# Kernel tuning notes

Measured on AMD Instinct MI355X. Metric: run time of the kernel, lower is better.

Reference implementation:

```python
import jax, jax.numpy as jnp
import numpy as np

N = 100000
E = 1600000
IN_C = 128
HID = 128
N_FACTORS = 3
N_SKILLS = 7
NEG_SLOPE = 0.2


def setup_inputs() -> dict:
    key = jax.random.key(0)
    ks = jax.random.split(key, 16)
    inp = {
        "x": jax.random.normal(ks[0], (N, IN_C), dtype=jnp.float32),
        "edge_index": jax.random.randint(ks[1], (2, E), 0, N, dtype=jnp.int64),
        # GAT layer 1
        "W1": jax.random.normal(ks[2], (HID, IN_C), dtype=jnp.float32) * (1.0 / np.sqrt(IN_C)),
        "a_src1": jax.random.normal(ks[3], (HID,), dtype=jnp.float32) * 0.1,
        "a_dst1": jax.random.normal(ks[4], (HID,), dtype=jnp.float32) * 0.1,
        "b1": jnp.zeros((HID,), dtype=jnp.float32),
        # GAT layer 2
        "W2": jax.random.normal(ks[5], (HID, HID), dtype=jnp.float32) * (1.0 / np.sqrt(HID)),
        "a_src2": jax.random.normal(ks[6], (HID,), dtype=jnp.float32) * 0.1,
        "a_dst2": jax.random.normal(ks[7], (HID,), dtype=jnp.float32) * 0.1,
        "b2": jnp.zeros((HID,), dtype=jnp.float32),
        # classifier heads
        "Wf": jax.random.normal(ks[8], (N_FACTORS, HID), dtype=jnp.float32) * (1.0 / np.sqrt(HID)),
        "bf": jnp.zeros((N_FACTORS,), dtype=jnp.float32),
        "Ws": jax.random.normal(ks[9], (N_SKILLS, HID), dtype=jnp.float32) * (1.0 / np.sqrt(HID)),
        "bs": jnp.zeros((N_SKILLS,), dtype=jnp.float32),
    }
    return inp


def _gat_layer(x, src, dst, W, a_src, a_dst, b):
    # x: [N, Fin] -> h: [N, Fout]; single-head GATConv (PyG defaults)
    n = x.shape[0]
    h = x @ W.T
    alpha_s = h @ a_src  # [N]
    alpha_d = h @ a_dst  # [N]
    e = jax.nn.leaky_relu(alpha_s[src] + alpha_d[dst], NEG_SLOPE)  # [E']
    # segment softmax over incoming edges of each dst node
    emax = jax.ops.segment_max(e, dst, num_segments=n)
    w = jnp.exp(e - emax[dst])
    denom = jax.ops.segment_sum(w, dst, num_segments=n)
    alpha = w / denom[dst]
    out = jax.ops.segment_sum(h[src] * alpha[:, None], dst, num_segments=n)
    return out + b


def reference(x, edge_index, W1, a_src1, a_dst1, b1, W2, a_src2, a_dst2, b2, Wf, bf, Ws, bs):
    # add self loops (PyG GATConv default add_self_loops=True)
    loops = jnp.arange(N, dtype=edge_index.dtype)
    src = jnp.concatenate([edge_index[0], loops])
    dst = jnp.concatenate([edge_index[1], loops])

    h = jax.nn.relu(_gat_layer(x, src, dst, W1, a_src1, a_dst1, b1))
    h = jax.nn.relu(_gat_layer(h, src, dst, W2, a_src2, a_dst2, b2))
    # dropout inactive in eval mode
    factors = h @ Wf.T + bf
    skills = h @ Ws.T + bs
    return (factors, skills)
```

## Files before the change

### kernel.cpp

```cpp
#include <hip/hip_runtime.h>
#include <hip/hip_bf16.h>
#include <hip/hip_fp16.h>
#include <math.h>

#define EPB 8192
#define BPB 256

typedef _Float16 v8h __attribute__((ext_vector_type(8)));
typedef float v4f __attribute__((ext_vector_type(4)));

__device__ inline float sum16(float v) {
#pragma unroll
  for (int off = 1; off < 16; off <<= 1) v += __shfl_xor(v, off);
  return v;
}

__device__ inline uint4 load8h(const float* p) {
  float4 a = *(const float4*)p;
  float4 b = *(const float4*)(p + 4);
  union { __half2 h[4]; uint4 u; } pk;
  pk.h[0] = __floats2half2_rn(a.x, a.y);
  pk.h[1] = __floats2half2_rn(a.z, a.w);
  pk.h[2] = __floats2half2_rn(b.x, b.y);
  pk.h[3] = __floats2half2_rn(b.z, b.w);
  return pk.u;
}
__device__ inline uint4 load8h(const __half* p) { return *(const uint4*)p; }

__global__ __launch_bounds__(256) void k_pcount(const int* __restrict__ ei,
                                                int* __restrict__ btot,
                                                int* __restrict__ blkoff,
                                                int nE, int n, int PB, int NB) {
  __shared__ int hist[512];
  int p = blockIdx.x, t = threadIdx.x;
  for (int i = t; i < NB; i += 256) hist[i] = 0;
  __syncthreads();
  int e0 = p * EPB;
  int e1 = min(e0 + EPB, nE);
  for (int i = e0 + t; i < e1; i += 256) {
    int d = ei[nE + i];
    if ((unsigned)d < (unsigned)n) atomicAdd(&hist[d >> 8], 1);
  }
  __syncthreads();
  for (int i = t; i < NB; i += 256) {
    int h = hist[i];
    int off = atomicAdd(&btot[i], h);
    blkoff[i * PB + p] = off;
  }
}

__global__ __launch_bounds__(256) void k_bscan(const int* __restrict__ btot,
                                               int* __restrict__ bbase, int NB) {
  __shared__ int s[256];
  int t = threadIdx.x;
  int v0 = (2 * t < NB) ? btot[2 * t] : 0;
  int v1 = (2 * t + 1 < NB) ? btot[2 * t + 1] : 0;
  int sum = v0 + v1;
  s[t] = sum;
  __syncthreads();
  for (int off = 1; off < 256; off <<= 1) {
    int x = (t >= off) ? s[t - off] : 0;
    __syncthreads();
    s[t] += x;
    __syncthreads();
  }
  int excl = s[t] - sum;
  if (2 * t < NB) bbase[2 * t] = excl;
  if (2 * t + 1 < NB) bbase[2 * t + 1] = excl + v0;
  if (t == 0) bbase[NB] = s[255];
}

__global__ __launch_bounds__(256) void k_ppart(const int* __restrict__ ei,
                                               const int* __restrict__ bbase,
                                               const int* __restrict__ blkoff,
                                               int2* __restrict__ part,
                                               int nE, int n, int PB, int NB) {
  __shared__ int cur[512];
  int p = blockIdx.x, t = threadIdx.x;
  for (int i = t; i < NB; i += 256) cur[i] = bbase[i] + blkoff[i * PB + p];
  __syncthreads();
  int e0 = p * EPB;
  int e1 = min(e0 + EPB, nE);
  for (int i = e0 + t; i < e1; i += 256) {
    int d = ei[nE + i];
    int s = ei[i];
    if ((unsigned)d < (unsigned)n) {
      int pos = atomicAdd(&cur[d >> 8], 1);
      part[pos] = make_int2(s, d);
    }
  }
}

__global__ __launch_bounds__(256) void k_bucket(const int2* __restrict__ part,
                                                const int* __restrict__ bbase,
                                                int* __restrict__ rowptr,
                                                int* __restrict__ col,
                                                int NB, int n) {
  __shared__ int sdeg[256];
  __shared__ int sscan[256];
  __shared__ int lcol[8448];
  int b = blockIdx.x, t = threadIdx.x;
  int node0 = b * BPB;
  int ebeg = bbase[b];
  int eend = bbase[b + 1];
  int cnt = eend - ebeg;
  if (cnt > 8192) cnt = 8192;
  int nloc = n - node0;
  if (nloc > BPB) nloc = BPB;

  sdeg[t] = (t < nloc) ? 1 : 0;
  __syncthreads();
  for (int i = t; i < cnt; i += 256) {
    int d = part[ebeg + i].y;
    atomicAdd(&sdeg[d - node0], 1);
  }
  __syncthreads();
  int v = sdeg[t];
  sscan[t] = v;
  __syncthreads();
  for (int off = 1; off < 256; off <<= 1) {
    int x = (t >= off) ? sscan[t - off] : 0;
    __syncthreads();
    sscan[t] += x;
    __syncthreads();
  }
  int excl = sscan[t] - v;
  int gbase = ebeg + node0;
  if (t < nloc) rowptr[node0 + t] = gbase + excl;
  if (b == NB - 1 && t == 0) rowptr[n] = bbase[NB] + n;
  if (t < nloc) lcol[excl] = node0 + t;
  sdeg[t] = excl + 1;
  __syncthreads();
  for (int i = t; i < cnt; i += 256) {
    int2 e = part[ebeg + i];
    int pos = atomicAdd(&sdeg[e.y - node0], 1);
    lcol[pos] = e.x;
  }
  __syncthreads();
  int T = cnt + nloc;
  for (int i = t; i < T; i += 256) col[gbase + i] = lcol[i];
}

template <typename T>
__global__ __launch_bounds__(256) void k_linear_mfma(const T* __restrict__ X,
                                                     const float* __restrict__ W,
                                                     const float* __restrict__ a_src,
                                                     const float* __restrict__ a_dst,
                                                     __half* __restrict__ H16,
                                                     float* __restrict__ as_,
                                                     float* __restrict__ ad_, int nrows) {
  __shared__ uint4 Xs[64 * 16];
  __shared__ uint4 Ws[128 * 16];
  int t = threadIdx.x;
  int row0 = blockIdx.x * 64;

#pragma unroll
  for (int i = 0; i < 4; ++i) {
    int idx = t + i * 256;
    int r = idx >> 4;
    int j = idx & 15;
    uint4 u = make_uint4(0u, 0u, 0u, 0u);
    if (row0 + r < nrows) u = load8h(&X[(size_t)(row0 + r) * 128 + j * 8]);
    Xs[r * 16 + (j ^ (r & 15))] = u;
  }
#pragma unroll
  for (int i = 0; i < 8; ++i) {
    int idx = t + i * 256;
    int c = idx >> 4;
    int j = idx & 15;
    Ws[c * 16 + (j ^ (c & 15))] = load8h(&W[(size_t)c * 128 + j * 8]);
  }
  __syncthreads();

  int w = t >> 6;
  int lane = t & 63;
  int li = lane & 15;
  int quad = lane >> 4;

  v4f acc[8];
#pragma unroll
  for (int ct = 0; ct < 8; ++ct) acc[ct] = (v4f){0.f, 0.f, 0.f, 0.f};

#pragma unroll
  for (int kk = 0; kk < 4; ++kk) {
    int ch = (kk * 4 + quad);
    union { uint4 u; v8h h; } av;
    av.u = Xs[(w * 16 + li) * 16 + (ch ^ li)];
#pragma unroll
    for (int ct = 0; ct < 8; ++ct) {
      union { uint4 u; v8h h; } bv;
      bv.u = Ws[(ct * 16 + li) * 16 + (ch ^ li)];
      acc[ct] = __builtin_amdgcn_mfma_f32_16x16x32_f16(av.h, bv.h, acc[ct], 0, 0, 0);
    }
  }

  float asum[4] = {0.f, 0.f, 0.f, 0.f};
  float adsum[4] = {0.f, 0.f, 0.f, 0.f};
#pragma unroll
  for (int ct = 0; ct < 8; ++ct) {
    float sa = a_src[ct * 16 + li];
    float da = a_dst[ct * 16 + li];
#pragma unroll
    for (int reg = 0; reg < 4; ++reg) {
      asum[reg] = fmaf(acc[ct][reg], sa, asum[reg]);
      adsum[reg] = fmaf(acc[ct][reg], da, adsum[reg]);
    }
  }
#pragma unroll
  for (int reg = 0; reg < 4; ++reg) {
    asum[reg] = sum16(asum[reg]);
    adsum[reg] = sum16(adsum[reg]);
  }
  if (li == 0) {
#pragma unroll
    for (int reg = 0; reg < 4; ++reg) {
      int r = row0 + w * 16 + quad * 4 + reg;
      if (r < nrows) {
        as_[r] = asum[reg];
        ad_[r] = adsum[reg];
      }
    }
  }

#pragma unroll
  for (int ct = 0; ct < 8; ++ct) {
#pragma unroll
    for (int reg = 0; reg < 4; ++reg) {
      float v0 = acc[ct][reg];
      float v1 = __shfl_xor(v0, 1);
      if (!(li & 1)) {
        int r = row0 + w * 16 + quad * 4 + reg;
        if (r < nrows) {
          __half2 hh = __floats2half2_rn(v0, v1);
          *(__half2*)&H16[(size_t)r * 128 + ct * 16 + li] = hh;
        }
      }
    }
  }
}

#define AGG_SLOT(K, QREG)                                                  \
  if (K == 0 || jj + K < trips) {                                          \
    float wj = __shfl(wgt, gb | (jj + K));                                 \
    uint4 cur = QREG;                                                      \
    if (jj + K + 4 < trips) {                                              \
      int sq = __shfl(s, gb | (jj + K + 4));                               \
      QREG = *(const uint4*)(h + (size_t)sq * 128 + li * 8);               \
    }                                                                      \
    float2 f0 = __half22float2(*(__half2*)&cur.x);                         \
    float2 f1 = __half22float2(*(__half2*)&cur.y);                         \
    float2 f2 = __half22float2(*(__half2*)&cur.z);                         \
    float2 f3 = __half22float2(*(__half2*)&cur.w);                         \
    acc0 = fmaf(f0.x, wj, acc0); acc1 = fmaf(f0.y, wj, acc1);              \
    acc2 = fmaf(f1.x, wj, acc2); acc3 = fmaf(f1.y, wj, acc3);              \
    acc4 = fmaf(f2.x, wj, acc4); acc5 = fmaf(f2.y, wj, acc5);              \
    acc6 = fmaf(f3.x, wj, acc6); acc7 = fmaf(f3.y, wj, acc7);              \
  }

template <bool HEADS>
__global__ __launch_bounds__(256) void k_agg_t(const __half* __restrict__ h,
                                               const float* __restrict__ as_,
                                               const float* __restrict__ ad_,
                                               const int* __restrict__ rowptr,
                                               const int* __restrict__ col,
                                               const float* __restrict__ bias,
                                               void* __restrict__ outp,
                                               const float* __restrict__ Wf,
                                               const float* __restrict__ bf,
                                               const float* __restrict__ Wsk,
                                               const float* __restrict__ bs,
                                               int n) {
  int gid = blockIdx.x * 256 + threadIdx.x;
  int wid = gid >> 6;
  int lane = gid & 63;
  int g = lane >> 4;
  int li = lane & 15;
  int gb = lane & 48;
  int node = wid * 4 + g;
  bool valid = node < n;
  int beg = 0, end = 0;
  float adv = 0.f;
  if (valid) {
    beg = rowptr[node];
    end = rowptr[node + 1];
    adv = ad_[node];
  }
  int deg = end - beg;
  int md = deg;
  md = max(md, __shfl_xor(md, 16));
  md = max(md, __shfl_xor(md, 32));

  float acc0 = 0.f, acc1 = 0.f, acc2 = 0.f, acc3 = 0.f;
  float acc4 = 0.f, acc5 = 0.f, acc6 = 0.f, acc7 = 0.f;
  float den_l = 0.f;

  for (int base = 0; base < md; base += 16) {
    int s = 0;
    float wgt = 0.f;
    if (base + li < deg) {
      s = col[beg + base + li];
      if ((unsigned)s >= (unsigned)n) s = 0;
      float v = as_[s] + adv;
      v = (v > 0.f) ? v : 0.2f * v;
      wgt = __expf(v);
    }
    den_l += wgt;

    int rem = md - base;
    int trips = rem > 16 ? 16 : rem;
    uint4 q0 = make_uint4(0u, 0u, 0u, 0u);
    uint4 q1 = q0, q2 = q0, q3 = q0;
    {
      int sq = __shfl(s, gb);
      q0 = *(const uint4*)(h + (size_t)sq * 128 + li * 8);
      if (trips > 1) { sq = __shfl(s, gb | 1); q1 = *(const uint4*)(h + (size_t)sq * 128 + li * 8); }
      if (trips > 2) { sq = __shfl(s, gb | 2); q2 = *(const uint4*)(h + (size_t)sq * 128 + li * 8); }
      if (trips > 3) { sq = __shfl(s, gb | 3); q3 = *(const uint4*)(h + (size_t)sq * 128 + li * 8); }
    }
    for (int jj = 0; jj < trips; jj += 4) {
      AGG_SLOT(0, q0)
      AGG_SLOT(1, q1)
      AGG_SLOT(2, q2)
      AGG_SLOT(3, q3)
    }
  }

  float den = sum16(den_l);
  float inv = 1.0f / den;

  float4 bv0 = *(const float4*)&bias[li * 8];
  float4 bv1 = *(const float4*)&bias[li * 8 + 4];
  float o0 = fmaxf(fmaf(acc0, inv, bv0.x), 0.f);
  float o1 = fmaxf(fmaf(acc1, inv, bv0.y), 0.f);
  float o2 = fmaxf(fmaf(acc2, inv, bv0.z), 0.f);
  float o3 = fmaxf(fmaf(acc3, inv, bv0.w), 0.f);
  float o4 = fmaxf(fmaf(acc4, inv, bv1.x), 0.f);
  float o5 = fmaxf(fmaf(acc5, inv, bv1.y), 0.f);
  float o6 = fmaxf(fmaf(acc6, inv, bv1.z), 0.f);
  float o7 = fmaxf(fmaf(acc7, inv, bv1.w), 0.f);

  if (!HEADS) {
    if (valid) {
      union { __half2 h2[4]; uint4 u; } pk;
      pk.h2[0] = __floats2half2_rn(o0, o1);
      pk.h2[1] = __floats2half2_rn(o2, o3);
      pk.h2[2] = __floats2half2_rn(o4, o5);
      pk.h2[3] = __floats2half2_rn(o6, o7);
      *(uint4*)&(((__half*)outp)[(size_t)node * 128 + li * 8]) = pk.u;
    }
  } else {
    float p[10];
#pragma unroll
    for (int j = 0; j < 3; ++j) {
      float4 w0 = *(const float4*)&Wf[(size_t)j * 128 + li * 8];
      float4 w1 = *(const float4*)&Wf[(size_t)j * 128 + li * 8 + 4];
      p[j] = o0 * w0.x + o1 * w0.y + o2 * w0.z + o3 * w0.w +
             o4 * w1.x + o5 * w1.y + o6 * w1.z + o7 * w1.w;
    }
#pragma unroll
    for (int j = 0; j < 7; ++j) {
      float4 w0 = *(const float4*)&Wsk[(size_t)j * 128 + li * 8];
      float4 w1 = *(const float4*)&Wsk[(size_t)j * 128 + li * 8 + 4];
      p[3 + j] = o0 * w0.x + o1 * w0.y + o2 * w0.z + o3 * w0.w +
                 o4 * w1.x + o5 * w1.y + o6 * w1.z + o7 * w1.w;
    }
#pragma unroll
    for (int j = 0; j < 10; ++j) p[j] = sum16(p[j]);
    if (li == 0 && valid) {
      float* out = (float*)outp;
#pragma unroll
      for (int j = 0; j < 3; ++j) out[(size_t)node * 3 + j] = p[j] + bf[j];
      float* sk = out + (size_t)n * 3;
#pragma unroll
      for (int j = 0; j < 7; ++j) sk[(size_t)node * 7 + j] = p[3 + j] + bs[j];
    }
  }
}

extern "C" void kernel_launch(void* const* d_in, const int* in_sizes, int n_in,
                              void* d_out, int out_size, void* d_ws, size_t ws_size,
                              hipStream_t stream) {
  const float* x = (const float*)d_in[0];
  const int* ei = (const int*)d_in[1];
  const float* W1 = (const float*)d_in[2];
  const float* a_src1 = (const float*)d_in[3];
  const float* a_dst1 = (const float*)d_in[4];
  const float* b1 = (const float*)d_in[5];
  const float* W2 = (const float*)d_in[6];
  const float* a_src2 = (const float*)d_in[7];
  const float* a_dst2 = (const float*)d_in[8];
  const float* b2 = (const float*)d_in[9];
  const float* Wf = (const float*)d_in[10];
  const float* bf = (const float*)d_in[11];
  const float* Wsk = (const float*)d_in[12];
  const float* bs = (const float*)d_in[13];
  float* out = (float*)d_out;

  const int N = in_sizes[0] / 128;
  const int nE = in_sizes[1] / 2;
  const int NB = (N + BPB - 1) / BPB;
  const int PB = (nE + EPB - 1) / EPB;
  const int NCNT = NB * PB;

  char* w = (char*)d_ws;
  auto carve = [&](size_t bytes) {
    char* p = w;
    w += (bytes + 255) & ~(size_t)255;
    return (void*)p;
  };
  __half* H16 = (__half*)carve((size_t)N * 128 * 2);
  __half* B16 = (__half*)carve((size_t)N * 128 * 2);
  float* as_ = (float*)carve((size_t)N * 4);
  float* ad_ = (float*)carve((size_t)N * 4);
  int* rowptr = (int*)carve((size_t)(N + 1) * 4);
  int* col = (int*)carve((size_t)(nE + N) * 4);
  int* btot = (int*)carve((size_t)(NB + 1) * 4);
  int* bbase = (int*)carve((size_t)(NB + 1) * 4);
  int* blkoff = (int*)carve((size_t)NCNT * 4);
  int2* part = (int2*)carve((size_t)nE * 8);

  dim3 b256(256);

  hipMemsetAsync(btot, 0, (size_t)(NB + 1) * 4, stream);
  k_pcount<<<PB, b256, 0, stream>>>(ei, btot, blkoff, nE, N, PB, NB);
  k_bscan<<<1, b256, 0, stream>>>(btot, bbase, NB);
  k_ppart<<<PB, b256, 0, stream>>>(ei, bbase, blkoff, part, nE, N, PB, NB);
  k_bucket<<<NB, b256, 0, stream>>>(part, bbase, rowptr, col, NB, N);

  const int gemm_blocks = (N + 63) / 64;
  const int agg_blocks = (((N + 3) / 4) * 64 + 255) / 256;

  k_linear_mfma<float><<<gemm_blocks, b256, 0, stream>>>(x, W1, a_src1, a_dst1, H16, as_, ad_, N);
  k_agg_t<false><<<agg_blocks, b256, 0, stream>>>(H16, as_, ad_, rowptr, col, b1, B16,
                                                  nullptr, nullptr, nullptr, nullptr, N);

  k_linear_mfma<__half><<<gemm_blocks, b256, 0, stream>>>(B16, W2, a_src2, a_dst2, H16, as_, ad_, N);
  k_agg_t<true><<<agg_blocks, b256, 0, stream>>>(H16, as_, ad_, rowptr, col, b2, out,
                                                 Wf, bf, Wsk, bs, N);
}
```

Baseline: 342.8 us.

## Slice feature matrix into 16-column panels and split GAT aggregation into edge-weight and sliced gather kernels

The hidden features are now stored as 8 column slices of 16 halves (32 bytes per node per slice), so each aggregation block gathers only one slice, which shrinks the random-access working set per pass for better cache reuse. Edge softmax weights and inverse denominators are precomputed in a separate kernel and written to memory. The output heads move into their own kernel. In exchange, col and rowptr are re-read for every slice, there are extra kernel launches, and an E-sized weight array must be written and read.

```diff
diff --git a/kernel.cpp b/kernel.cpp
--- a/kernel.cpp
+++ b/kernel.cpp
@@ -25,7 +25,6 @@
   pk.h[3] = __floats2half2_rn(b.z, b.w);
   return pk.u;
 }
-__device__ inline uint4 load8h(const __half* p) { return *(const uint4*)p; }
 
 __global__ __launch_bounds__(256) void k_pcount(const int* __restrict__ ei,
                                                 int* __restrict__ btot,
@@ -141,7 +140,7 @@
   for (int i = t; i < T; i += 256) col[gbase + i] = lcol[i];
 }
 
-template <typename T>
+template <typename T, bool SLICED_IN>
 __global__ __launch_bounds__(256) void k_linear_mfma(const T* __restrict__ X,
                                                      const float* __restrict__ W,
                                                      const float* __restrict__ a_src,
@@ -160,7 +159,15 @@
     int r = idx >> 4;
     int j = idx & 15;
     uint4 u = make_uint4(0u, 0u, 0u, 0u);
-    if (row0 + r < nrows) u = load8h(&X[(size_t)(row0 + r) * 128 + j * 8]);
+    int rr = row0 + r;
+    if (rr < nrows) {
+      if (SLICED_IN) {
+        const __half* Xh = (const __half*)X;
+        u = *(const uint4*)&Xh[((size_t)(j >> 1) * nrows + rr) * 16 + (j & 1) * 8];
+      } else {
+        u = load8h((const float*)X + (size_t)rr * 128 + j * 8);
+      }
+    }
     Xs[r * 16 + (j ^ (r & 15))] = u;
   }
 #pragma unroll
@@ -183,7 +190,7 @@
 
 #pragma unroll
   for (int kk = 0; kk < 4; ++kk) {
-    int ch = (kk * 4 + quad);
+    int ch = kk * 4 + quad;
     union { uint4 u; v8h h; } av;
     av.u = Xs[(w * 16 + li) * 16 + (ch ^ li)];
 #pragma unroll
@@ -232,50 +239,24 @@
         int r = row0 + w * 16 + quad * 4 + reg;
         if (r < nrows) {
           __half2 hh = __floats2half2_rn(v0, v1);
-          *(__half2*)&H16[(size_t)r * 128 + ct * 16 + li] = hh;
+          *(__half2*)&H16[((size_t)ct * nrows + r) * 16 + li] = hh;
         }
       }
     }
   }
 }
 
-#define AGG_SLOT(K, QREG)                                                  \
-  if (K == 0 || jj + K < trips) {                                          \
-    float wj = __shfl(wgt, gb | (jj + K));                                 \
-    uint4 cur = QREG;                                                      \
-    if (jj + K + 4 < trips) {                                              \
-      int sq = __shfl(s, gb | (jj + K + 4));                               \
-      QREG = *(const uint4*)(h + (size_t)sq * 128 + li * 8);               \
-    }                                                                      \
-    float2 f0 = __half22float2(*(__half2*)&cur.x);                         \
-    float2 f1 = __half22float2(*(__half2*)&cur.y);                         \
-    float2 f2 = __half22float2(*(__half2*)&cur.z);                         \
-    float2 f3 = __half22float2(*(__half2*)&cur.w);                         \
-    acc0 = fmaf(f0.x, wj, acc0); acc1 = fmaf(f0.y, wj, acc1);              \
-    acc2 = fmaf(f1.x, wj, acc2); acc3 = fmaf(f1.y, wj, acc3);              \
-    acc4 = fmaf(f2.x, wj, acc4); acc5 = fmaf(f2.y, wj, acc5);              \
-    acc6 = fmaf(f3.x, wj, acc6); acc7 = fmaf(f3.y, wj, acc7);              \
-  }
-
-template <bool HEADS>
-__global__ __launch_bounds__(256) void k_agg_t(const __half* __restrict__ h,
-                                               const float* __restrict__ as_,
+__global__ __launch_bounds__(256) void k_edgew(const float* __restrict__ as_,
                                                const float* __restrict__ ad_,
                                                const int* __restrict__ rowptr,
                                                const int* __restrict__ col,
-                                               const float* __restrict__ bias,
-                                               void* __restrict__ outp,
-                                               const float* __restrict__ Wf,
-                                               const float* __restrict__ bf,
-                                               const float* __restrict__ Wsk,
-                                               const float* __restrict__ bs,
-                                               int n) {
+                                               float* __restrict__ wexp,
+                                               float* __restrict__ deninv, int n) {
   int gid = blockIdx.x * 256 + threadIdx.x;
   int wid = gid >> 6;
   int lane = gid & 63;
   int g = lane >> 4;
   int li = lane & 15;
-  int gb = lane & 48;
   int node = wid * 4 + g;
   bool valid = node < n;
   int beg = 0, end = 0;
@@ -286,94 +267,143 @@
     adv = ad_[node];
   }
   int deg = end - beg;
-  int md = deg;
-  md = max(md, __shfl_xor(md, 16));
-  md = max(md, __shfl_xor(md, 32));
-
-  float acc0 = 0.f, acc1 = 0.f, acc2 = 0.f, acc3 = 0.f;
-  float acc4 = 0.f, acc5 = 0.f, acc6 = 0.f, acc7 = 0.f;
   float den_l = 0.f;
-
-  for (int base = 0; base < md; base += 16) {
+  for (int j = li; j < deg; j += 16) {
+    int s = col[beg + j];
+    if ((unsigned)s >= (unsigned)n) s = 0;
+    float v = as_[s] + adv;
+    v = (v > 0.f) ? v : 0.2f * v;
+    float wv = __expf(v);
+    wexp[beg + j] = wv;
+    den_l += wv;
+  }
+  float den = sum16(den_l);
+  if (li == 0 && valid) deninv[node] = 1.0f / den;
+}
+
+__global__ __launch_bounds__(256) void k_agg_slice(const __half* __restrict__ Hs,
+                                                   const float* __restrict__ wexp,
+                                                   const float* __restrict__ deninv,
+                                                   const int* __restrict__ rowptr,
+                                                   const int* __restrict__ col,
+                                                   const float* __restrict__ bias,
+                                                   __half* __restrict__ Os, int n) {
+  int slice = blockIdx.x & 7;
+  int nb = blockIdx.x >> 3;
+  int w = threadIdx.x >> 6;
+  int lane = threadIdx.x & 63;
+  int g = lane >> 4;
+  int li = lane & 15;
+  int p = li & 1;
+  int q = li >> 1;
+  int node = nb * 16 + w * 4 + g;
+  bool valid = node < n;
+  int beg = 0, end = 0;
+  if (valid) {
+    beg = rowptr[node];
+    end = rowptr[node + 1];
+  }
+  int deg = end - beg;
+  const __half* hsl = Hs + (size_t)slice * n * 16;
+
+  float acc[8];
+#pragma unroll
+  for (int k = 0; k < 8; ++k) acc[k] = 0.f;
+
+  for (int base = 0; base < deg; base += 8) {
+    int j = base + q;
     int s = 0;
     float wgt = 0.f;
-    if (base + li < deg) {
-      s = col[beg + base + li];
+    if (j < deg) {
+      s = col[beg + j];
       if ((unsigned)s >= (unsigned)n) s = 0;
-      float v = as_[s] + adv;
-      v = (v > 0.f) ? v : 0.2f * v;
-      wgt = __expf(v);
-    }
-    den_l += wgt;
-
-    int rem = md - base;
-    int trips = rem > 16 ? 16 : rem;
-    uint4 q0 = make_uint4(0u, 0u, 0u, 0u);
-    uint4 q1 = q0, q2 = q0, q3 = q0;
-    {
-      int sq = __shfl(s, gb);
-      q0 = *(const uint4*)(h + (size_t)sq * 128 + li * 8);
-      if (trips > 1) { sq = __shfl(s, gb | 1); q1 = *(const uint4*)(h + (size_t)sq * 128 + li * 8); }
-      if (trips > 2) { sq = __shfl(s, gb | 2); q2 = *(const uint4*)(h + (size_t)sq * 128 + li * 8); }
-      if (trips > 3) { sq = __shfl(s, gb | 3); q3 = *(const uint4*)(h + (size_t)sq * 128 + li * 8); }
-    }
-    for (int jj = 0; jj < trips; jj += 4) {
-      AGG_SLOT(0, q0)
-      AGG_SLOT(1, q1)
-      AGG_SLOT(2, q2)
-      AGG_SLOT(3, q3)
-    }
-  }
-
-  float den = sum16(den_l);
-  float inv = 1.0f / den;
-
-  float4 bv0 = *(const float4*)&bias[li * 8];
-  float4 bv1 = *(const float4*)&bias[li * 8 + 4];
-  float o0 = fmaxf(fmaf(acc0, inv, bv0.x), 0.f);
-  float o1 = fmaxf(fmaf(acc1, inv, bv0.y), 0.f);
-  float o2 = fmaxf(fmaf(acc2, inv, bv0.z), 0.f);
-  float o3 = fmaxf(fmaf(acc3, inv, bv0.w), 0.f);
-  float o4 = fmaxf(fmaf(acc4, inv, bv1.x), 0.f);
-  float o5 = fmaxf(fmaf(acc5, inv, bv1.y), 0.f);
-  float o6 = fmaxf(fmaf(acc6, inv, bv1.z), 0.f);
-  float o7 = fmaxf(fmaf(acc7, inv, bv1.w), 0.f);
-
-  if (!HEADS) {
-    if (valid) {
-      union { __half2 h2[4]; uint4 u; } pk;
-      pk.h2[0] = __floats2half2_rn(o0, o1);
-      pk.h2[1] = __floats2half2_rn(o2, o3);
-      pk.h2[2] = __floats2half2_rn(o4, o5);
-      pk.h2[3] = __floats2half2_rn(o6, o7);
-      *(uint4*)&(((__half*)outp)[(size_t)node * 128 + li * 8]) = pk.u;
-    }
-  } else {
-    float p[10];
-#pragma unroll
-    for (int j = 0; j < 3; ++j) {
-      float4 w0 = *(const float4*)&Wf[(size_t)j * 128 + li * 8];
-      float4 w1 = *(const float4*)&Wf[(size_t)j * 128 + li * 8 + 4];
-      p[j] = o0 * w0.x + o1 * w0.y + o2 * w0.z + o3 * w0.w +
-             o4 * w1.x + o5 * w1.y + o6 * w1.z + o7 * w1.w;
-    }
-#pragma unroll
-    for (int j = 0; j < 7; ++j) {
-      float4 w0 = *(const float4*)&Wsk[(size_t)j * 128 + li * 8];
-      float4 w1 = *(const float4*)&Wsk[(size_t)j * 128 + li * 8 + 4];
-      p[3 + j] = o0 * w0.x + o1 * w0.y + o2 * w0.z + o3 * w0.w +
-                 o4 * w1.x + o5 * w1.y + o6 * w1.z + o7 * w1.w;
-    }
-#pragma unroll
-    for (int j = 0; j < 10; ++j) p[j] = sum16(p[j]);
-    if (li == 0 && valid) {
-      float* out = (float*)outp;
-#pragma unroll
-      for (int j = 0; j < 3; ++j) out[(size_t)node * 3 + j] = p[j] + bf[j];
-      float* sk = out + (size_t)n * 3;
-#pragma unroll
-      for (int j = 0; j < 7; ++j) sk[(size_t)node * 7 + j] = p[3 + j] + bs[j];
-    }
+      wgt = wexp[beg + j];
+    }
+    uint4 hv = *(const uint4*)(hsl + (size_t)s * 16 + p * 8);
+    float2 f0 = __half22float2(*(__half2*)&hv.x);
+    float2 f1 = __half22float2(*(__half2*)&hv.y);
+    float2 f2 = __half22float2(*(__half2*)&hv.z);
+    float2 f3 = __half22float2(*(__half2*)&hv.w);
+    acc[0] = fmaf(f0.x, wgt, acc[0]);
+    acc[1] = fmaf(f0.y, wgt, acc[1]);
+    acc[2] = fmaf(f1.x, wgt, acc[2]);
+    acc[3] = fmaf(f1.y, wgt, acc[3]);
+    acc[4] = fmaf(f2.x, wgt, acc[4]);
+    acc[5] = fmaf(f2.y, wgt, acc[5]);
+    acc[6] = fmaf(f3.x, wgt, acc[6]);
+    acc[7] = fmaf(f3.y, wgt, acc[7]);
+  }
+
+#pragma unroll
+  for (int off = 2; off <= 8; off <<= 1) {
+#pragma unroll
+    for (int k = 0; k < 8; ++k) acc[k] += __shfl_xor(acc[k], off);
+  }
+
+  float inv = valid ? deninv[node] : 0.f;
+  int c0 = slice * 16 + p * 8;
+  float4 b0 = *(const float4*)&bias[c0];
+  float4 b1 = *(const float4*)&bias[c0 + 4];
+  float o0 = fmaxf(fmaf(acc[0], inv, b0.x), 0.f);
+  float o1 = fmaxf(fmaf(acc[1], inv, b0.y), 0.f);
+  float o2 = fmaxf(fmaf(acc[2], inv, b0.z), 0.f);
+  float o3 = fmaxf(fmaf(acc[3], inv, b0.w), 0.f);
+  float o4 = fmaxf(fmaf(acc[4], inv, b1.x), 0.f);
+  float o5 = fmaxf(fmaf(acc[5], inv, b1.y), 0.f);
+  float o6 = fmaxf(fmaf(acc[6], inv, b1.z), 0.f);
+  float o7 = fmaxf(fmaf(acc[7], inv, b1.w), 0.f);
+
+  if (li < 2 && valid) {
+    union { __half2 h2[4]; uint4 u; } pk;
+    pk.h2[0] = __floats2half2_rn(o0, o1);
+    pk.h2[1] = __floats2half2_rn(o2, o3);
+    pk.h2[2] = __floats2half2_rn(o4, o5);
+    pk.h2[3] = __floats2half2_rn(o6, o7);
+    *(uint4*)&Os[((size_t)slice * n + node) * 16 + p * 8] = pk.u;
+  }
+}
+
+__global__ __launch_bounds__(256) void k_heads(const __half* __restrict__ Fs,
+                                               const float* __restrict__ Wf,
+                                               const float* __restrict__ bf,
+                                               const float* __restrict__ Wsk,
+                                               const float* __restrict__ bs,
+                                               float* __restrict__ out, int n) {
+  int gid = blockIdx.x * 256 + threadIdx.x;
+  int wid = gid >> 6;
+  int lane = gid & 63;
+  int g = lane >> 4;
+  int li = lane & 15;
+  int node = wid * 4 + g;
+  if (node >= n) return;
+  uint4 hv = *(const uint4*)&Fs[((size_t)(li >> 1) * n + node) * 16 + (li & 1) * 8];
+  float2 f0 = __half22float2(*(__half2*)&hv.x);
+  float2 f1 = __half22float2(*(__half2*)&hv.y);
+  float2 f2 = __half22float2(*(__half2*)&hv.z);
+  float2 f3 = __half22float2(*(__half2*)&hv.w);
+  float p[10];
+#pragma unroll
+  for (int j = 0; j < 3; ++j) {
+    float4 w0 = *(const float4*)&Wf[(size_t)j * 128 + li * 8];
+    float4 w1 = *(const float4*)&Wf[(size_t)j * 128 + li * 8 + 4];
+    p[j] = f0.x * w0.x + f0.y * w0.y + f1.x * w0.z + f1.y * w0.w +
+           f2.x * w1.x + f2.y * w1.y + f3.x * w1.z + f3.y * w1.w;
+  }
+#pragma unroll
+  for (int j = 0; j < 7; ++j) {
+    float4 w0 = *(const float4*)&Wsk[(size_t)j * 128 + li * 8];
+    float4 w1 = *(const float4*)&Wsk[(size_t)j * 128 + li * 8 + 4];
+    p[3 + j] = f0.x * w0.x + f0.y * w0.y + f1.x * w0.z + f1.y * w0.w +
+               f2.x * w1.x + f2.y * w1.y + f3.x * w1.z + f3.y * w1.w;
+  }
+#pragma unroll
+  for (int j = 0; j < 10; ++j) p[j] = sum16(p[j]);
+  if (li == 0) {
+#pragma unroll
+    for (int j = 0; j < 3; ++j) out[(size_t)node * 3 + j] = p[j] + bf[j];
+    float* sk = out + (size_t)n * 3;
+#pragma unroll
+    for (int j = 0; j < 7; ++j) sk[(size_t)node * 7 + j] = p[3 + j] + bs[j];
   }
 }
 
@@ -412,6 +442,8 @@
   __half* B16 = (__half*)carve((size_t)N * 128 * 2);
   float* as_ = (float*)carve((size_t)N * 4);
   float* ad_ = (float*)carve((size_t)N * 4);
+  float* deninv = (float*)carve((size_t)N * 4);
+  float* wexp = (float*)carve((size_t)(nE + N) * 4);
   int* rowptr = (int*)carve((size_t)(N + 1) * 4);
   int* col = (int*)carve((size_t)(nE + N) * 4);
   int* btot = (int*)carve((size_t)(NB + 1) * 4);
@@ -428,13 +460,18 @@
   k_bucket<<<NB, b256, 0, stream>>>(part, bbase, rowptr, col, NB, N);
 
   const int gemm_blocks = (N + 63) / 64;
-  const int agg_blocks = (((N + 3) / 4) * 64 + 255) / 256;
-
-  k_linear_mfma<float><<<gemm_blocks, b256, 0, stream>>>(x, W1, a_src1, a_dst1, H16, as_, ad_, N);
-  k_agg_t<false><<<agg_blocks, b256, 0, stream>>>(H16, as_, ad_, rowptr, col, b1, B16,
-                                                  nullptr, nullptr, nullptr, nullptr, N);
-
-  k_linear_mfma<__half><<<gemm_blocks, b256, 0, stream>>>(B16, W2, a_src2, a_dst2, H16, as_, ad_, N);
-  k_agg_t<true><<<agg_blocks, b256, 0, stream>>>(H16, as_, ad_, rowptr, col, b2, out,
-                                                 Wf, bf, Wsk, bs, N);
-}
+  const int nodewave_blocks = (((N + 3) / 4) * 64 + 255) / 256;
+  const int agg_blocks = ((N + 15) / 16) * 8;
+
+  k_linear_mfma<float, false><<<gemm_blocks, b256, 0, stream>>>(x, W1, a_src1, a_dst1,
+                                                                H16, as_, ad_, N);
+  k_edgew<<<nodewave_blocks, b256, 0, stream>>>(as_, ad_, rowptr, col, wexp, deninv, N);
+  k_agg_slice<<<agg_blocks, b256, 0, stream>>>(H16, wexp, deninv, rowptr, col, b1, B16, N);
+
+  k_linear_mfma<__half, true><<<gemm_blocks, b256, 0, stream>>>((const __half*)B16, W2,
+                                                                a_src2, a_dst2, H16, as_, ad_, N);
+  k_edgew<<<nodewave_blocks, b256, 0, stream>>>(as_, ad_, rowptr, col, wexp, deninv, N);
+  k_agg_slice<<<agg_blocks, b256, 0, stream>>>(H16, wexp, deninv, rowptr, col, b2, B16, N);
+
+  k_heads<<<nodewave_blocks, b256, 0, stream>>>(B16, Wf, bf, Wsk, bs, out, N);
+}
```

Measured after the change: 450.2 us. +31.3%, slower.

## Sort nodes by degree for aggregation load balance and pack partition entries

Applied to the files above, without the earlier changes.

Adds a counting sort of nodes by in-degree (histogram, scan and scatter kernels) that writes a permutation. Both aggregation kernels then map each 16-lane group to a node through it, so the four nodes sharing a wavefront have similar degree and less lane idling on the max-degree loop. The edge partition buffer is also packed from int2 to a single 32-bit word (source shifted left by 8 bits plus the local destination index), halving that traffic. The price is three extra small kernel launches and scattered output writes and rowptr reads in aggregation, and the packing assumes node ids fit in 24 bits.

```diff
diff --git a/kernel.cpp b/kernel.cpp
--- a/kernel.cpp
+++ b/kernel.cpp
@@ -5,6 +5,7 @@
 
 #define EPB 8192
 #define BPB 256
+#define DBLK 1024
 
 typedef _Float16 v8h __attribute__((ext_vector_type(8)));
 typedef float v4f __attribute__((ext_vector_type(4)));
@@ -73,7 +74,7 @@
 __global__ __launch_bounds__(256) void k_ppart(const int* __restrict__ ei,
                                                const int* __restrict__ bbase,
                                                const int* __restrict__ blkoff,
-                                               int2* __restrict__ part,
+                                               unsigned* __restrict__ part,
                                                int nE, int n, int PB, int NB) {
   __shared__ int cur[512];
   int p = blockIdx.x, t = threadIdx.x;
@@ -86,15 +87,16 @@
     int s = ei[i];
     if ((unsigned)d < (unsigned)n) {
       int pos = atomicAdd(&cur[d >> 8], 1);
-      part[pos] = make_int2(s, d);
-    }
-  }
-}
-
-__global__ __launch_bounds__(256) void k_bucket(const int2* __restrict__ part,
+      part[pos] = ((unsigned)s << 8) | (unsigned)(d & 255);
+    }
+  }
+}
+
+__global__ __launch_bounds__(256) void k_bucket(const unsigned* __restrict__ part,
                                                 const int* __restrict__ bbase,
                                                 int* __restrict__ rowptr,
                                                 int* __restrict__ col,
+                                                int* __restrict__ deg_arr,
                                                 int NB, int n) {
   __shared__ int sdeg[256];
   __shared__ int sscan[256];
@@ -111,8 +113,8 @@
   sdeg[t] = (t < nloc) ? 1 : 0;
   __syncthreads();
   for (int i = t; i < cnt; i += 256) {
-    int d = part[ebeg + i].y;
-    atomicAdd(&sdeg[d - node0], 1);
+    int dl = part[ebeg + i] & 255u;
+    atomicAdd(&sdeg[dl], 1);
   }
   __syncthreads();
   int v = sdeg[t];
@@ -126,19 +128,69 @@
   }
   int excl = sscan[t] - v;
   int gbase = ebeg + node0;
-  if (t < nloc) rowptr[node0 + t] = gbase + excl;
+  if (t < nloc) {
+    rowptr[node0 + t] = gbase + excl;
+    deg_arr[node0 + t] = v;
+  }
   if (b == NB - 1 && t == 0) rowptr[n] = bbase[NB] + n;
   if (t < nloc) lcol[excl] = node0 + t;
   sdeg[t] = excl + 1;
   __syncthreads();
   for (int i = t; i < cnt; i += 256) {
-    int2 e = part[ebeg + i];
-    int pos = atomicAdd(&sdeg[e.y - node0], 1);
-    lcol[pos] = e.x;
+    unsigned e = part[ebeg + i];
+    int pos = atomicAdd(&sdeg[e & 255u], 1);
+    lcol[pos] = (int)(e >> 8);
   }
   __syncthreads();
   int T = cnt + nloc;
   for (int i = t; i < T; i += 256) col[gbase + i] = lcol[i];
+}
+
+__global__ __launch_bounds__(256) void k_dhist(const int* __restrict__ deg,
+                                               int* __restrict__ dbin,
+                                               int* __restrict__ dblk, int n, int NBd) {
+  __shared__ int hist[256];
+  int b = blockIdx.x, t = threadIdx.x;
+  hist[t] = 0;
+  __syncthreads();
+  int i0 = b * DBLK, i1 = min(i0 + DBLK, n);
+  for (int i = i0 + t; i < i1; i += 256) atomicAdd(&hist[min(deg[i], 255)], 1);
+  __syncthreads();
+  int c = hist[t];
+  int off = 0;
+  if (c) off = atomicAdd(&dbin[t], c);
+  dblk[t * NBd + b] = off;
+}
+
+__global__ __launch_bounds__(256) void k_dscan(const int* __restrict__ dbin,
+                                               int* __restrict__ dbase) {
+  __shared__ int s[256];
+  int t = threadIdx.x;
+  int v = dbin[255 - t];
+  s[t] = v;
+  __syncthreads();
+  for (int off = 1; off < 256; off <<= 1) {
+    int x = (t >= off) ? s[t - off] : 0;
+    __syncthreads();
+    s[t] += x;
+    __syncthreads();
+  }
+  dbase[255 - t] = s[t] - v;
+}
+
+__global__ __launch_bounds__(256) void k_dscatter(const int* __restrict__ deg,
+                                                  const int* __restrict__ dbase,
+                                                  const int* __restrict__ dblk,
+                                                  int* __restrict__ perm, int n, int NBd) {
+  __shared__ int cur[256];
+  int b = blockIdx.x, t = threadIdx.x;
+  cur[t] = dbase[t] + dblk[t * NBd + b];
+  __syncthreads();
+  int i0 = b * DBLK, i1 = min(i0 + DBLK, n);
+  for (int i = i0 + t; i < i1; i += 256) {
+    int pos = atomicAdd(&cur[min(deg[i], 255)], 1);
+    perm[pos] = i;
+  }
 }
 
 template <typename T>
@@ -183,7 +235,7 @@
 
 #pragma unroll
   for (int kk = 0; kk < 4; ++kk) {
-    int ch = (kk * 4 + quad);
+    int ch = kk * 4 + quad;
     union { uint4 u; v8h h; } av;
     av.u = Xs[(w * 16 + li) * 16 + (ch ^ li)];
 #pragma unroll
@@ -263,6 +315,7 @@
                                                const float* __restrict__ ad_,
                                                const int* __restrict__ rowptr,
                                                const int* __restrict__ col,
+                                               const int* __restrict__ perm,
                                                const float* __restrict__ bias,
                                                void* __restrict__ outp,
                                                const float* __restrict__ Wf,
@@ -276,7 +329,8 @@
   int g = lane >> 4;
   int li = lane & 15;
   int gb = lane & 48;
-  int node = wid * 4 + g;
+  int idx = wid * 4 + g;
+  int node = (idx < n) ? perm[idx] : n;
   bool valid = node < n;
   int beg = 0, end = 0;
   float adv = 0.f;
@@ -401,6 +455,7 @@
   const int NB = (N + BPB - 1) / BPB;
   const int PB = (nE + EPB - 1) / EPB;
   const int NCNT = NB * PB;
+  const int NBd = (N + DBLK - 1) / DBLK;
 
   char* w = (char*)d_ws;
   auto carve = [&](size_t bytes) {
@@ -414,27 +469,37 @@
   float* ad_ = (float*)carve((size_t)N * 4);
   int* rowptr = (int*)carve((size_t)(N + 1) * 4);
   int* col = (int*)carve((size_t)(nE + N) * 4);
-  int* btot = (int*)carve((size_t)(NB + 1) * 4);
+  int* deg_arr = (int*)carve((size_t)N * 4);
+  int* perm = (int*)carve((size_t)N * 4);
+  int* zeros = (int*)carve((size_t)(NB + 1 + 256) * 4);
+  int* btot = zeros;
+  int* dbin = zeros + NB + 1;
   int* bbase = (int*)carve((size_t)(NB + 1) * 4);
+  int* dbase = (int*)carve(256 * 4);
   int* blkoff = (int*)carve((size_t)NCNT * 4);
-  int2* part = (int2*)carve((size_t)nE * 8);
+  int* dblk = (int*)carve((size_t)256 * NBd * 4);
+  unsigned* part = (unsigned*)carve((size_t)nE * 4);
 
   dim3 b256(256);
 
-  hipMemsetAsync(btot, 0, (size_t)(NB + 1) * 4, stream);
+  hipMemsetAsync(zeros, 0, (size_t)(NB + 1 + 256) * 4, stream);
   k_pcount<<<PB, b256, 0, stream>>>(ei, btot, blkoff, nE, N, PB, NB);
   k_bscan<<<1, b256, 0, stream>>>(btot, bbase, NB);
   k_ppart<<<PB, b256, 0, stream>>>(ei, bbase, blkoff, part, nE, N, PB, NB);
-  k_bucket<<<NB, b256, 0, stream>>>(part, bbase, rowptr, col, NB, N);
+  k_bucket<<<NB, b256, 0, stream>>>(part, bbase, rowptr, col, deg_arr, NB, N);
+
+  k_dhist<<<NBd, b256, 0, stream>>>(deg_arr, dbin, dblk, N, NBd);
+  k_dscan<<<1, b256, 0, stream>>>(dbin, dbase);
+  k_dscatter<<<NBd, b256, 0, stream>>>(deg_arr, dbase, dblk, perm, N, NBd);
 
   const int gemm_blocks = (N + 63) / 64;
   const int agg_blocks = (((N + 3) / 4) * 64 + 255) / 256;
 
   k_linear_mfma<float><<<gemm_blocks, b256, 0, stream>>>(x, W1, a_src1, a_dst1, H16, as_, ad_, N);
-  k_agg_t<false><<<agg_blocks, b256, 0, stream>>>(H16, as_, ad_, rowptr, col, b1, B16,
+  k_agg_t<false><<<agg_blocks, b256, 0, stream>>>(H16, as_, ad_, rowptr, col, perm, b1, B16,
                                                   nullptr, nullptr, nullptr, nullptr, N);
 
   k_linear_mfma<__half><<<gemm_blocks, b256, 0, stream>>>(B16, W2, a_src2, a_dst2, H16, as_, ad_, N);
-  k_agg_t<true><<<agg_blocks, b256, 0, stream>>>(H16, as_, ad_, rowptr, col, b2, out,
+  k_agg_t<true><<<agg_blocks, b256, 0, stream>>>(H16, as_, ad_, rowptr, col, perm, b2, out,
                                                  Wf, bf, Wsk, bs, N);
 }
```

Result: slower. 350.0 us (+2.1%).

## Fuse edge count with layer-1 GEMM, drop scan kernel, pack partition entries

Applied to the files above, without the earlier changes.

The edge-histogram pass and the first-layer MFMA GEMM now run as one launch, with block IDs split between the two roles so both proceed concurrently. The separate single-block scan kernel is removed; the partition and bucket kernels each redo a 512-entry prefix scan of the bucket totals in shared memory. Partition entries are packed into one 32-bit word (source shifted left by 8, local destination in the low byte) instead of an int2, halving that buffer's traffic. This trades two launches and a serial dependency for redundant per-block scan work and a 48KB static shared allocation in the fused and GEMM kernels, which may lower occupancy.

```diff
diff --git a/kernel.cpp b/kernel.cpp
--- a/kernel.cpp
+++ b/kernel.cpp
@@ -27,12 +27,29 @@
 }
 __device__ inline uint4 load8h(const __half* p) { return *(const uint4*)p; }
 
-__global__ __launch_bounds__(256) void k_pcount(const int* __restrict__ ei,
-                                                int* __restrict__ btot,
-                                                int* __restrict__ blkoff,
-                                                int nE, int n, int PB, int NB) {
-  __shared__ int hist[512];
-  int p = blockIdx.x, t = threadIdx.x;
+__device__ inline int* scan_inc512(const int* __restrict__ btot, int NB, int t,
+                                   int* sA, int* sB) {
+#pragma unroll
+  for (int i = t; i < 512; i += 256) sA[i] = (i < NB) ? btot[i] : 0;
+  __syncthreads();
+  int* src = sA;
+  int* dst = sB;
+  for (int off = 1; off < 512; off <<= 1) {
+#pragma unroll
+    for (int i = t; i < 512; i += 256) {
+      int v = src[i];
+      if (i >= off) v += src[i - off];
+      dst[i] = v;
+    }
+    __syncthreads();
+    int* tmp = src; src = dst; dst = tmp;
+  }
+  return src;
+}
+
+__device__ inline void pcount_body(const int* __restrict__ ei, int* __restrict__ btot,
+                                   int* __restrict__ blkoff, int* hist,
+                                   int p, int t, int nE, int n, int PB, int NB) {
   for (int i = t; i < NB; i += 256) hist[i] = 0;
   __syncthreads();
   int e0 = p * EPB;
@@ -49,111 +66,14 @@
   }
 }
 
-__global__ __launch_bounds__(256) void k_bscan(const int* __restrict__ btot,
-                                               int* __restrict__ bbase, int NB) {
-  __shared__ int s[256];
-  int t = threadIdx.x;
-  int v0 = (2 * t < NB) ? btot[2 * t] : 0;
-  int v1 = (2 * t + 1 < NB) ? btot[2 * t + 1] : 0;
-  int sum = v0 + v1;
-  s[t] = sum;
-  __syncthreads();
-  for (int off = 1; off < 256; off <<= 1) {
-    int x = (t >= off) ? s[t - off] : 0;
-    __syncthreads();
-    s[t] += x;
-    __syncthreads();
-  }
-  int excl = s[t] - sum;
-  if (2 * t < NB) bbase[2 * t] = excl;
-  if (2 * t + 1 < NB) bbase[2 * t + 1] = excl + v0;
-  if (t == 0) bbase[NB] = s[255];
-}
-
-__global__ __launch_bounds__(256) void k_ppart(const int* __restrict__ ei,
-                                               const int* __restrict__ bbase,
-                                               const int* __restrict__ blkoff,
-                                               int2* __restrict__ part,
-                                               int nE, int n, int PB, int NB) {
-  __shared__ int cur[512];
-  int p = blockIdx.x, t = threadIdx.x;
-  for (int i = t; i < NB; i += 256) cur[i] = bbase[i] + blkoff[i * PB + p];
-  __syncthreads();
-  int e0 = p * EPB;
-  int e1 = min(e0 + EPB, nE);
-  for (int i = e0 + t; i < e1; i += 256) {
-    int d = ei[nE + i];
-    int s = ei[i];
-    if ((unsigned)d < (unsigned)n) {
-      int pos = atomicAdd(&cur[d >> 8], 1);
-      part[pos] = make_int2(s, d);
-    }
-  }
-}
-
-__global__ __launch_bounds__(256) void k_bucket(const int2* __restrict__ part,
-                                                const int* __restrict__ bbase,
-                                                int* __restrict__ rowptr,
-                                                int* __restrict__ col,
-                                                int NB, int n) {
-  __shared__ int sdeg[256];
-  __shared__ int sscan[256];
-  __shared__ int lcol[8448];
-  int b = blockIdx.x, t = threadIdx.x;
-  int node0 = b * BPB;
-  int ebeg = bbase[b];
-  int eend = bbase[b + 1];
-  int cnt = eend - ebeg;
-  if (cnt > 8192) cnt = 8192;
-  int nloc = n - node0;
-  if (nloc > BPB) nloc = BPB;
-
-  sdeg[t] = (t < nloc) ? 1 : 0;
-  __syncthreads();
-  for (int i = t; i < cnt; i += 256) {
-    int d = part[ebeg + i].y;
-    atomicAdd(&sdeg[d - node0], 1);
-  }
-  __syncthreads();
-  int v = sdeg[t];
-  sscan[t] = v;
-  __syncthreads();
-  for (int off = 1; off < 256; off <<= 1) {
-    int x = (t >= off) ? sscan[t - off] : 0;
-    __syncthreads();
-    sscan[t] += x;
-    __syncthreads();
-  }
-  int excl = sscan[t] - v;
-  int gbase = ebeg + node0;
-  if (t < nloc) rowptr[node0 + t] = gbase + excl;
-  if (b == NB - 1 && t == 0) rowptr[n] = bbase[NB] + n;
-  if (t < nloc) lcol[excl] = node0 + t;
-  sdeg[t] = excl + 1;
-  __syncthreads();
-  for (int i = t; i < cnt; i += 256) {
-    int2 e = part[ebeg + i];
-    int pos = atomicAdd(&sdeg[e.y - node0], 1);
-    lcol[pos] = e.x;
-  }
-  __syncthreads();
-  int T = cnt + nloc;
-  for (int i = t; i < T; i += 256) col[gbase + i] = lcol[i];
-}
-
 template <typename T>
-__global__ __launch_bounds__(256) void k_linear_mfma(const T* __restrict__ X,
-                                                     const float* __restrict__ W,
-                                                     const float* __restrict__ a_src,
-                                                     const float* __restrict__ a_dst,
-                                                     __half* __restrict__ H16,
-                                                     float* __restrict__ as_,
-                                                     float* __restrict__ ad_, int nrows) {
-  __shared__ uint4 Xs[64 * 16];
-  __shared__ uint4 Ws[128 * 16];
-  int t = threadIdx.x;
-  int row0 = blockIdx.x * 64;
-
+__device__ inline void gemm_tile(uint4* Xs, uint4* Ws, int t, int row0,
+                                 const T* __restrict__ X, const float* __restrict__ W,
+                                 const float* __restrict__ a_src,
+                                 const float* __restrict__ a_dst,
+                                 __half* __restrict__ H16,
+                                 float* __restrict__ as_, float* __restrict__ ad_,
+                                 int nrows) {
 #pragma unroll
   for (int i = 0; i < 4; ++i) {
     int idx = t + i * 256;
@@ -183,7 +103,7 @@
 
 #pragma unroll
   for (int kk = 0; kk < 4; ++kk) {
-    int ch = (kk * 4 + quad);
+    int ch = kk * 4 + quad;
     union { uint4 u; v8h h; } av;
     av.u = Xs[(w * 16 + li) * 16 + (ch ^ li)];
 #pragma unroll
@@ -237,6 +157,123 @@
       }
     }
   }
+}
+
+__global__ __launch_bounds__(256) void k_fused1(const int* __restrict__ ei,
+                                                int* __restrict__ btot,
+                                                int* __restrict__ blkoff,
+                                                int nE, int n, int PB, int NB,
+                                                const float* __restrict__ X,
+                                                const float* __restrict__ W,
+                                                const float* __restrict__ a_src,
+                                                const float* __restrict__ a_dst,
+                                                __half* __restrict__ H16,
+                                                float* __restrict__ as_,
+                                                float* __restrict__ ad_) {
+  __shared__ __align__(16) char smraw[48 * 1024];
+  int t = threadIdx.x;
+  if ((int)blockIdx.x < PB) {
+    pcount_body(ei, btot, blkoff, (int*)smraw, blockIdx.x, t, nE, n, PB, NB);
+  } else {
+    uint4* Xs = (uint4*)smraw;
+    uint4* Ws = (uint4*)(smraw + 16384);
+    int row0 = (blockIdx.x - PB) * 64;
+    gemm_tile<float>(Xs, Ws, t, row0, X, W, a_src, a_dst, H16, as_, ad_, n);
+  }
+}
+
+__global__ __launch_bounds__(256) void k_linear2(const __half* __restrict__ X,
+                                                 const float* __restrict__ W,
+                                                 const float* __restrict__ a_src,
+                                                 const float* __restrict__ a_dst,
+                                                 __half* __restrict__ H16,
+                                                 float* __restrict__ as_,
+                                                 float* __restrict__ ad_, int nrows) {
+  __shared__ __align__(16) char smraw[48 * 1024];
+  uint4* Xs = (uint4*)smraw;
+  uint4* Ws = (uint4*)(smraw + 16384);
+  gemm_tile<__half>(Xs, Ws, threadIdx.x, blockIdx.x * 64, X, W, a_src, a_dst,
+                    H16, as_, ad_, nrows);
+}
+
+__global__ __launch_bounds__(256) void k_ppart(const int* __restrict__ ei,
+                                               const int* __restrict__ btot,
+                                               const int* __restrict__ blkoff,
+                                               unsigned* __restrict__ part,
+                                               int nE, int n, int PB, int NB) {
+  __shared__ int sA[512], sB[512];
+  __shared__ int cur[512];
+  int p = blockIdx.x, t = threadIdx.x;
+  int* inc = scan_inc512(btot, NB, t, sA, sB);
+  for (int i = t; i < NB; i += 256) {
+    int excl = (i == 0) ? 0 : inc[i - 1];
+    cur[i] = excl + blkoff[i * PB + p];
+  }
+  __syncthreads();
+  int e0 = p * EPB;
+  int e1 = min(e0 + EPB, nE);
+  for (int i = e0 + t; i < e1; i += 256) {
+    int d = ei[nE + i];
+    int s = ei[i];
+    if ((unsigned)d < (unsigned)n) {
+      int pos = atomicAdd(&cur[d >> 8], 1);
+      part[pos] = ((unsigned)s << 8) | (unsigned)(d & 255);
+    }
+  }
+}
+
+__global__ __launch_bounds__(256) void k_bucket(const unsigned* __restrict__ part,
+                                                const int* __restrict__ btot,
+                                                int* __restrict__ rowptr,
+                                                int* __restrict__ col,
+                                                int NB, int n) {
+  __shared__ int sdeg[256];
+  __shared__ int sscan[256];
+  __shared__ int lcol[8448];
+  int b = blockIdx.x, t = threadIdx.x;
+  int node0 = b * BPB;
+  int* inc = scan_inc512(btot, NB, t, lcol, lcol + 512);
+  int ebeg = (b == 0) ? 0 : inc[b - 1];
+  int eend = inc[b];
+  int total = inc[NB - 1];
+  __syncthreads();
+
+  int cnt = eend - ebeg;
+  if (cnt > 8192) cnt = 8192;
+  int nloc = n - node0;
+  if (nloc > BPB) nloc = BPB;
+
+  sdeg[t] = (t < nloc) ? 1 : 0;
+  __syncthreads();
+  for (int i = t; i < cnt; i += 256) {
+    int dl = part[ebeg + i] & 255u;
+    atomicAdd(&sdeg[dl], 1);
+  }
+  __syncthreads();
+  int v = sdeg[t];
+  sscan[t] = v;
+  __syncthreads();
+  for (int off = 1; off < 256; off <<= 1) {
+    int x = (t >= off) ? sscan[t - off] : 0;
+    __syncthreads();
+    sscan[t] += x;
+    __syncthreads();
+  }
+  int excl = sscan[t] - v;
+  int gbase = ebeg + node0;
+  if (t < nloc) rowptr[node0 + t] = gbase + excl;
+  if (b == NB - 1 && t == 0) rowptr[n] = total + n;
+  if (t < nloc) lcol[excl] = node0 + t;
+  sdeg[t] = excl + 1;
+  __syncthreads();
+  for (int i = t; i < cnt; i += 256) {
+    unsigned e = part[ebeg + i];
+    int pos = atomicAdd(&sdeg[e & 255u], 1);
+    lcol[pos] = (int)(e >> 8);
+  }
+  __syncthreads();
+  int T = cnt + nloc;
+  for (int i = t; i < T; i += 256) col[gbase + i] = lcol[i];
 }
 
 #define AGG_SLOT(K, QREG)                                                  \
@@ -415,26 +452,23 @@
   int* rowptr = (int*)carve((size_t)(N + 1) * 4);
   int* col = (int*)carve((size_t)(nE + N) * 4);
   int* btot = (int*)carve((size_t)(NB + 1) * 4);
-  int* bbase = (int*)carve((size_t)(NB + 1) * 4);
   int* blkoff = (int*)carve((size_t)NCNT * 4);
-  int2* part = (int2*)carve((size_t)nE * 8);
+  unsigned* part = (unsigned*)carve((size_t)nE * 4);
 
   dim3 b256(256);
-
-  hipMemsetAsync(btot, 0, (size_t)(NB + 1) * 4, stream);
-  k_pcount<<<PB, b256, 0, stream>>>(ei, btot, blkoff, nE, N, PB, NB);
-  k_bscan<<<1, b256, 0, stream>>>(btot, bbase, NB);
-  k_ppart<<<PB, b256, 0, stream>>>(ei, bbase, blkoff, part, nE, N, PB, NB);
-  k_bucket<<<NB, b256, 0, stream>>>(part, bbase, rowptr, col, NB, N);
-
   const int gemm_blocks = (N + 63) / 64;
   const int agg_blocks = (((N + 3) / 4) * 64 + 255) / 256;
 
-  k_linear_mfma<float><<<gemm_blocks, b256, 0, stream>>>(x, W1, a_src1, a_dst1, H16, as_, ad_, N);
+  hipMemsetAsync(btot, 0, (size_t)(NB + 1) * 4, stream);
+  k_fused1<<<PB + gemm_blocks, b256, 0, stream>>>(ei, btot, blkoff, nE, N, PB, NB,
+                                                  x, W1, a_src1, a_dst1, H16, as_, ad_);
+  k_ppart<<<PB, b256, 0, stream>>>(ei, btot, blkoff, part, nE, N, PB, NB);
+  k_bucket<<<NB, b256, 0, stream>>>(part, btot, rowptr, col, NB, N);
+
   k_agg_t<false><<<agg_blocks, b256, 0, stream>>>(H16, as_, ad_, rowptr, col, b1, B16,
                                                   nullptr, nullptr, nullptr, nullptr, N);
 
-  k_linear_mfma<__half><<<gemm_blocks, b256, 0, stream>>>(B16, W2, a_src2, a_dst2, H16, as_, ad_, N);
+  k_linear2<<<gemm_blocks, b256, 0, stream>>>(B16, W2, a_src2, a_dst2, H16, as_, ad_, N);
   k_agg_t<true><<<agg_blocks, b256, 0, stream>>>(H16, as_, ad_, rowptr, col, b2, out,
                                                  Wf, bf, Wsk, bs, N);
 }
```

New measurement: 341.0 us. No clear change (-0.5%).
